# Kernel tuning notes

Hardware: AMD Instinct MI355X
Metric: run time of the kernel (lower is better)

Reference implementation:

```python
import jax, jax.numpy as jnp
import numpy as np

DIM = 2048
NUM_HEADS = 16
HEAD_DIM = 128
INNER = NUM_HEADS * HEAD_DIM


def rotate_half(x):
    x1, x2 = jnp.split(x, 2, axis=-1)
    return jnp.concatenate([-x2, x1], axis=-1)


def rope_tables(T, head_dim):
    inv_freq = 1.0 / (10000.0 ** (np.arange(0, head_dim, 2, dtype=np.float32) / head_dim))
    t = np.arange(T, dtype=np.float32)
    freqs = np.einsum('i,j->ij', t, inv_freq)  # [T, hd/2]
    emb = np.concatenate([freqs, freqs], axis=-1)  # [T, hd]
    return jnp.asarray(np.cos(emb)), jnp.asarray(np.sin(emb))


def setup_inputs() -> dict:
    key = jax.random.key(0)
    k1, k2, k3 = jax.random.split(key, 3)
    B, T = 2, 2048
    x = jax.random.normal(k1, (B, T, DIM), dtype=jnp.float32)
    scale = 1.0 / np.sqrt(DIM)
    w_qkv = jax.random.normal(k2, (DIM, 3 * INNER), dtype=jnp.float32) * scale
    w_out = jax.random.normal(k3, (INNER, DIM), dtype=jnp.float32) * (1.0 / np.sqrt(INNER))
    return {"x": x, "w_qkv": w_qkv, "w_out": w_out}


def reference(x, w_qkv, w_out):
    B, T, _ = x.shape
    qkv = x @ w_qkv  # [B, T, 3*INNER]
    q, k, v = jnp.split(qkv, 3, axis=-1)
    # [B, H, T, hd]
    q = q.reshape(B, T, NUM_HEADS, HEAD_DIM).transpose(0, 2, 1, 3)
    k = k.reshape(B, T, NUM_HEADS, HEAD_DIM).transpose(0, 2, 1, 3)
    v = v.reshape(B, T, NUM_HEADS, HEAD_DIM).transpose(0, 2, 1, 3)
    cos, sin = rope_tables(T, HEAD_DIM)  # [T, hd]
    cos = cos[None, None]
    sin = sin[None, None]
    q = q * cos + rotate_half(q) * sin
    k = k * cos + rotate_half(k) * sin
    # causal SDPA
    scale = 1.0 / np.sqrt(HEAD_DIM)
    scores = jnp.einsum('bhqd,bhkd->bhqk', q, k) * scale
    mask = jnp.tril(jnp.ones((T, T), dtype=bool))
    scores = jnp.where(mask[None, None], scores, jnp.finfo(scores.dtype).min)
    attn = jax.nn.softmax(scores, axis=-1)
    out = jnp.einsum('bhqk,bhkd->bhqd', attn, v)
    out = out.transpose(0, 2, 1, 3).reshape(B, T, INNER)
    return out @ w_out
```

## Files before the change

kernel.cpp:

```cpp
#include <hip/hip_runtime.h>
#include <hip/hip_bf16.h>
#include <math.h>

typedef __bf16 bf16x8 __attribute__((ext_vector_type(8)));
typedef float f32x4 __attribute__((ext_vector_type(4)));
typedef unsigned short ushort8_t __attribute__((ext_vector_type(8)));

#define DIMSZ 2048
#define NHEADS 16
#define HD 128
#define INNER 2048
#define T_SEQ 2048
#define BATCH 2
#define BT_ROWS (BATCH * T_SEQ)
#define QKV_COLS (3 * INNER)

__device__ __forceinline__ float bf2f(unsigned short u) {
  union { unsigned int ui; float f; } v; v.ui = ((unsigned int)u) << 16; return v.f;
}
__device__ __forceinline__ unsigned short f2bf(float f) {
  union { float f; unsigned int ui; } v; v.f = f;
  unsigned int u = v.ui;
  return (unsigned short)((u + 0x7FFFu + ((u >> 16) & 1u)) >> 16);
}
__device__ __forceinline__ bf16x8 ld8(const unsigned short* p) {
  return *(const bf16x8*)p;
}
__device__ __forceinline__ void gl16(const unsigned short* g, unsigned short* l) {
  __builtin_amdgcn_global_load_lds(
      (const __attribute__((address_space(1))) unsigned int*)g,
      (__attribute__((address_space(3))) unsigned int*)l, 16, 0, 0);
}

__global__ void detect_dtype(const unsigned short* __restrict__ w, int* __restrict__ flag) {
  __shared__ int sh;
  if (threadIdx.x == 0) sh = 0;
  __syncthreads();
  int hit = 0;
  for (int i = threadIdx.x; i < 8192; i += 256) {
    unsigned int e = (w[i] >> 7) & 0xFF;
    if (e >= 0x7F) hit = 1;
  }
  if (hit) atomicOr(&sh, 1);
  __syncthreads();
  if (threadIdx.x == 0) *flag = sh;
}

__global__ void convert_x(const void* __restrict__ in, unsigned short* __restrict__ out,
                          const int* __restrict__ flag) {
  const bool f32 = (*flag != 0);
  size_t i = ((size_t)blockIdx.x * 256 + threadIdx.x) * 8;
  if (f32) {
    const float* inf = (const float*)in;
    float4 u0 = *(const float4*)&inf[i];
    float4 u1 = *(const float4*)&inf[i + 4];
    ushort8_t t;
    t[0] = f2bf(u0.x); t[1] = f2bf(u0.y); t[2] = f2bf(u0.z); t[3] = f2bf(u0.w);
    t[4] = f2bf(u1.x); t[5] = f2bf(u1.y); t[6] = f2bf(u1.z); t[7] = f2bf(u1.w);
    *(ushort8_t*)&out[i] = t;
  } else {
    *(uint4*)&out[i] = *(const uint4*)&((const unsigned short*)in)[i];
  }
}

__global__ void transpose_any(const void* __restrict__ in, unsigned short* __restrict__ out,
                              int R, int C, const int* __restrict__ flag) {
  const bool f32 = (*flag != 0);
  __shared__ unsigned short tile[32][33];
  int c0 = blockIdx.x * 32, r0 = blockIdx.y * 32;
  int tx = threadIdx.x & 31, ty = threadIdx.x >> 5;
  if (f32) {
    const float* inf = (const float*)in;
    #pragma unroll
    for (int i = 0; i < 4; ++i)
      tile[ty + i * 8][tx] = f2bf(inf[(size_t)(r0 + ty + i * 8) * C + c0 + tx]);
  } else {
    const unsigned short* inu = (const unsigned short*)in;
    #pragma unroll
    for (int i = 0; i < 4; ++i)
      tile[ty + i * 8][tx] = inu[(size_t)(r0 + ty + i * 8) * C + c0 + tx];
  }
  __syncthreads();
  #pragma unroll
  for (int i = 0; i < 4; ++i)
    out[(size_t)(c0 + ty + i * 8) * R + r0 + tx] = tile[tx][ty + i * 8];
}

__global__ __launch_bounds__(256) void gemm_lds(const unsigned short* __restrict__ A,
                                                const unsigned short* __restrict__ Bt,
                                                unsigned short* __restrict__ Cb,
                                                float* __restrict__ Cf,
                                                int M, int N, int K) {
  __shared__ unsigned short As[128 * 32];
  __shared__ unsigned short Bs[128 * 32];
  const int tid = threadIdx.x;
  const int m0 = blockIdx.y * 128, n0 = blockIdx.x * 128;
  const int w = tid >> 6, L = tid & 63, lane = tid & 63, c = lane & 15, quad = lane >> 4;
  const int wm = (w & 1) * 64, wn = (w >> 1) * 64;
  f32x4 acc[4][4];
  #pragma unroll
  for (int i = 0; i < 4; ++i)
    #pragma unroll
    for (int j = 0; j < 4; ++j) acc[i][j] = (f32x4)0.0f;

  for (int k0 = 0; k0 < K; k0 += 32) {
    #pragma unroll
    for (int p = 0; p < 2; ++p) {
      int ci = p * 256 + w * 64 + L;
      int r = ci >> 2, s = ci & 3;
      gl16(&A[(size_t)(m0 + r) * K + k0 + s * 8], &As[(size_t)(p * 256 + w * 64) * 8]);
      gl16(&Bt[(size_t)(n0 + r) * K + k0 + s * 8], &Bs[(size_t)(p * 256 + w * 64) * 8]);
    }
    __syncthreads();
    bf16x8 af[4], bfr[4];
    #pragma unroll
    for (int i = 0; i < 4; ++i) af[i] = ld8(&As[(wm + i * 16 + c) * 32 + quad * 8]);
    #pragma unroll
    for (int j = 0; j < 4; ++j) bfr[j] = ld8(&Bs[(wn + j * 16 + c) * 32 + quad * 8]);
    #pragma unroll
    for (int i = 0; i < 4; ++i)
      #pragma unroll
      for (int j = 0; j < 4; ++j)
        acc[i][j] = __builtin_amdgcn_mfma_f32_16x16x32_bf16(af[i], bfr[j], acc[i][j], 0, 0, 0);
    __syncthreads();
  }
  if (Cf) {
    #pragma unroll
    for (int i = 0; i < 4; ++i)
      #pragma unroll
      for (int j = 0; j < 4; ++j)
        #pragma unroll
        for (int r = 0; r < 4; ++r)
          Cf[(size_t)(m0 + wm + i * 16 + quad * 4 + r) * N + n0 + wn + j * 16 + c] = acc[i][j][r];
  } else {
    #pragma unroll
    for (int i = 0; i < 4; ++i)
      #pragma unroll
      for (int j = 0; j < 4; ++j)
        #pragma unroll
        for (int r = 0; r < 4; ++r)
          Cb[(size_t)(m0 + wm + i * 16 + quad * 4 + r) * N + n0 + wn + j * 16 + c] =
              f2bf(acc[i][j][r]);
  }
}

__global__ void rope_kernel(unsigned short* __restrict__ qkv) {
  int idx = blockIdx.x * 256 + threadIdx.x;
  int jb = (idx & 7) * 8;
  int head = (idx >> 3) & 15;
  int qk = (idx >> 7) & 1;
  int row = idx >> 8;
  int t = row & (T_SEQ - 1);
  size_t base = (size_t)row * QKV_COLS + qk * INNER + head * HD + jb;
  ushort8_t x1 = *(ushort8_t*)&qkv[base];
  ushort8_t x2 = *(ushort8_t*)&qkv[base + 64];
  ushort8_t o1, o2;
  #pragma unroll
  for (int e = 0; e < 8; ++e) {
    float inv_freq = exp2f(-(float)(jb + e) * 0.20762050593046017f);
    float ang = (float)t * inv_freq;
    float sn = sinf(ang), cs = cosf(ang);
    float a = bf2f(x1[e]), bq = bf2f(x2[e]);
    o1[e] = f2bf(a * cs - bq * sn);
    o2[e] = f2bf(bq * cs + a * sn);
  }
  *(ushort8_t*)&qkv[base] = o1;
  *(ushort8_t*)&qkv[base + 64] = o2;
}

#define KT 64
#define KSTR 136
#define VSTR 72
#define PSTR 72
__global__ __launch_bounds__(256) void flash_attn2(const unsigned short* __restrict__ qkv,
                                                   unsigned short* __restrict__ aout) {
  __shared__ unsigned short Ks[KT * KSTR];
  __shared__ unsigned short Vs[HD * VSTR];
  __shared__ unsigned short Ps[4 * 16 * PSTR];
  const int tid = threadIdx.x, wave = tid >> 6, lane = tid & 63, c = lane & 15, quad = lane >> 4;
  const int bh = blockIdx.y, b = bh >> 4, h = bh & 15;
  unsigned short* myPs = &Ps[wave * 16 * PSTR];
  const unsigned short* qbase = qkv + (size_t)b * T_SEQ * QKV_COLS + h * HD;
  const unsigned short* kbase = qbase + INNER;
  const unsigned short* vbase = qbase + 2 * INNER;
  const float cf = 0.12751743f;

  for (int half = 0; half < 2; ++half) {
    const int qt = (half == 0) ? (int)blockIdx.x : 31 - (int)blockIdx.x;
    const int q0 = qt * 64;
    const int qrow = q0 + wave * 16;

    bf16x8 aq[4];
    #pragma unroll
    for (int ch = 0; ch < 4; ++ch)
      aq[ch] = ld8(&qbase[(size_t)(qrow + c) * QKV_COLS + ch * 32 + quad * 8]);

    f32x4 o[8];
    #pragma unroll
    for (int t = 0; t < 8; ++t) o[t] = (f32x4)0.0f;
    float l_part[4] = {0.f, 0.f, 0.f, 0.f};

    const int nkt = qt + 1;
    for (int it = 0; it < nkt; ++it) {
      const int kt = it * KT;
      __syncthreads();
      #pragma unroll
      for (int p = 0; p < 4; ++p) {
        int ci = p * 256 + tid;
        int r = ci >> 4, s = ci & 15;
        *(uint4*)&Ks[r * KSTR + s * 8] = *(const uint4*)&kbase[(size_t)(kt + r) * QKV_COLS + s * 8];
      }
      {
        int rp = tid & 31, seg = tid >> 5;
        const unsigned short* vp = &vbase[(size_t)(kt + 2 * rp) * QKV_COLS + seg * 16];
        ushort8_t v0a = *(const ushort8_t*)vp;
        ushort8_t v0b = *(const ushort8_t*)(vp + 8);
        ushort8_t v1a = *(const ushort8_t*)(vp + QKV_COLS);
        ushort8_t v1b = *(const ushort8_t*)(vp + QKV_COLS + 8);
        #pragma unroll
        for (int e = 0; e < 8; ++e) {
          *(unsigned int*)&Vs[(seg * 16 + e) * VSTR + 2 * rp] =
              (unsigned int)v0a[e] | ((unsigned int)v1a[e] << 16);
          *(unsigned int*)&Vs[(seg * 16 + 8 + e) * VSTR + 2 * rp] =
              (unsigned int)v0b[e] | ((unsigned int)v1b[e] << 16);
        }
      }
      __syncthreads();

      f32x4 s[4];
      #pragma unroll
      for (int st = 0; st < 4; ++st) s[st] = (f32x4)0.0f;
      #pragma unroll
      for (int ch = 0; ch < 4; ++ch) {
        #pragma unroll
        for (int st = 0; st < 4; ++st) {
          bf16x8 kf = ld8(&Ks[(st * 16 + c) * KSTR + ch * 32 + quad * 8]);
          s[st] = __builtin_amdgcn_mfma_f32_16x16x32_bf16(aq[ch], kf, s[st], 0, 0, 0);
        }
      }
      #pragma unroll
      for (int st = 0; st < 4; ++st) {
        #pragma unroll
        for (int r = 0; r < 4; ++r) {
          int qg = qrow + quad * 4 + r;
          int kg = kt + st * 16 + c;
          float p = (kg <= qg) ? exp2f(s[st][r] * cf) : 0.0f;
          l_part[r] += p;
          myPs[(quad * 4 + r) * PSTR + st * 16 + c] = f2bf(p);
        }
      }
      __syncthreads();
      bf16x8 pf0 = ld8(&myPs[c * PSTR + quad * 8]);
      bf16x8 pf1 = ld8(&myPs[c * PSTR + 32 + quad * 8]);
      #pragma unroll
      for (int t = 0; t < 8; ++t) {
        bf16x8 vf0 = ld8(&Vs[(t * 16 + c) * VSTR + quad * 8]);
        bf16x8 vf1 = ld8(&Vs[(t * 16 + c) * VSTR + 32 + quad * 8]);
        o[t] = __builtin_amdgcn_mfma_f32_16x16x32_bf16(pf0, vf0, o[t], 0, 0, 0);
        o[t] = __builtin_amdgcn_mfma_f32_16x16x32_bf16(pf1, vf1, o[t], 0, 0, 0);
      }
    }
    float inv[4];
    #pragma unroll
    for (int r = 0; r < 4; ++r) {
      float v = l_part[r];
      #pragma unroll
      for (int off = 1; off <= 8; off <<= 1) v += __shfl_xor(v, off, 64);
      inv[r] = 1.0f / v;
    }
    #pragma unroll
    for (int t = 0; t < 8; ++t)
      #pragma unroll
      for (int r = 0; r < 4; ++r)
        aout[(size_t)((size_t)b * T_SEQ + qrow + quad * 4 + r) * INNER + h * HD + t * 16 + c] =
            f2bf(o[t][r] * inv[r]);
  }
}

extern "C" void kernel_launch(void* const* d_in, const int* in_sizes, int n_in,
                              void* d_out, int out_size, void* d_ws, size_t ws_size,
                              hipStream_t stream) {
  const void* x     = d_in[0];
  const void* w_qkv = d_in[1];
  const void* w_out = d_in[2];
  float* out = (float*)d_out;

  int* flag = (int*)d_ws;
  unsigned short* qkvbuf  = (unsigned short*)((char*)d_ws + 256);
  unsigned short* attnout = qkvbuf + (size_t)BT_ROWS * QKV_COLS;
  unsigned short* wqkvT   = attnout + (size_t)BT_ROWS * INNER;
  unsigned short* woutT   = wqkvT + (size_t)QKV_COLS * DIMSZ;
  unsigned short* xb      = woutT + (size_t)DIMSZ * INNER;

  detect_dtype<<<1, 256, 0, stream>>>((const unsigned short*)w_qkv, flag);
  convert_x<<<dim3((size_t)BT_ROWS * DIMSZ / 2048), 256, 0, stream>>>(x, xb, flag);
  transpose_any<<<dim3(QKV_COLS / 32, DIMSZ / 32), 256, 0, stream>>>(w_qkv, wqkvT, DIMSZ, QKV_COLS, flag);
  transpose_any<<<dim3(DIMSZ / 32, INNER / 32), 256, 0, stream>>>(w_out, woutT, INNER, DIMSZ, flag);
  gemm_lds<<<dim3(QKV_COLS / 128, BT_ROWS / 128), 256, 0, stream>>>(xb, wqkvT, qkvbuf, nullptr, BT_ROWS, QKV_COLS, DIMSZ);
  rope_kernel<<<dim3(BT_ROWS * NHEADS * 2 * 8 / 256), 256, 0, stream>>>(qkvbuf);
  flash_attn2<<<dim3(16, BATCH * NHEADS), 256, 0, stream>>>(qkvbuf, attnout);
  gemm_lds<<<dim3(DIMSZ / 128, BT_ROWS / 128), 256, 0, stream>>>(attnout, woutT, nullptr, out, BT_ROWS, DIMSZ, INNER);
}
```

Baseline: 474.3 us.

## Rewrite flash attention with 32x32 MFMA tiles and split-K wave partitioning

Replaces the 16x16x32 MFMA attention kernel with one using 32x32x16 MFMAs, where the four waves form a 2x2 grid over query rows and key halves of each 64-key tile. Partial outputs and row sums from the two key-half waves are combined through shared memory at the end. The goal is fewer MFMA instructions and less LDS fragment traffic per tile, and removing the per-tile barrier before the P·V step. The cost is an extra reduction pass through LDS and more accumulator registers, with the launch bound set to 2 blocks.

```diff
diff --git a/kernel.cpp b/kernel.cpp
--- a/kernel.cpp
+++ b/kernel.cpp
@@ -4,7 +4,9 @@
 
 typedef __bf16 bf16x8 __attribute__((ext_vector_type(8)));
 typedef float f32x4 __attribute__((ext_vector_type(4)));
+typedef float f32x16 __attribute__((ext_vector_type(16)));
 typedef unsigned short ushort8_t __attribute__((ext_vector_type(8)));
+typedef unsigned short ushort4_t __attribute__((ext_vector_type(4)));
 
 #define DIMSZ 2048
 #define NHEADS 16
@@ -168,18 +170,27 @@
   *(ushort8_t*)&qkv[base + 64] = o2;
 }
 
-#define KT 64
-#define KSTR 136
-#define VSTR 72
-#define PSTR 72
-__global__ __launch_bounds__(256) void flash_attn2(const unsigned short* __restrict__ qkv,
-                                                   unsigned short* __restrict__ aout) {
-  __shared__ unsigned short Ks[KT * KSTR];
-  __shared__ unsigned short Vs[HD * VSTR];
-  __shared__ unsigned short Ps[4 * 16 * PSTR];
-  const int tid = threadIdx.x, wave = tid >> 6, lane = tid & 63, c = lane & 15, quad = lane >> 4;
+#define KT3 64
+#define KSTR3 136
+#define VSTR3 72
+#define PSTR3 68
+#define SM_VS (64 * KSTR3 * 2)
+#define SM_PS (SM_VS + 128 * VSTR3 * 2)
+#define SM_LR (SM_PS + 64 * PSTR3 * 2)
+#define SM_TOT (SM_LR + 2 * 64 * 4)
+__global__ __launch_bounds__(256, 2) void flash_attn3(const unsigned short* __restrict__ qkv,
+                                                      unsigned short* __restrict__ aout) {
+  __shared__ char smem[SM_TOT];
+  unsigned short* Ks = (unsigned short*)smem;
+  unsigned short* Vs = (unsigned short*)(smem + SM_VS);
+  unsigned short* Ps = (unsigned short*)(smem + SM_PS);
+  float* lred = (float*)(smem + SM_LR);
+  float* Os = (float*)smem;
+
+  const int tid = threadIdx.x, wave = tid >> 6, lane = tid & 63;
+  const int wq = wave & 1, wk = wave >> 1;
+  const int l31 = lane & 31, lh = lane >> 5;
   const int bh = blockIdx.y, b = bh >> 4, h = bh & 15;
-  unsigned short* myPs = &Ps[wave * 16 * PSTR];
   const unsigned short* qbase = qkv + (size_t)b * T_SEQ * QKV_COLS + h * HD;
   const unsigned short* kbase = qbase + INNER;
   const unsigned short* vbase = qbase + 2 * INNER;
@@ -188,27 +199,26 @@
   for (int half = 0; half < 2; ++half) {
     const int qt = (half == 0) ? (int)blockIdx.x : 31 - (int)blockIdx.x;
     const int q0 = qt * 64;
-    const int qrow = q0 + wave * 16;
-
-    bf16x8 aq[4];
-    #pragma unroll
-    for (int ch = 0; ch < 4; ++ch)
-      aq[ch] = ld8(&qbase[(size_t)(qrow + c) * QKV_COLS + ch * 32 + quad * 8]);
-
-    f32x4 o[8];
-    #pragma unroll
-    for (int t = 0; t < 8; ++t) o[t] = (f32x4)0.0f;
-    float l_part[4] = {0.f, 0.f, 0.f, 0.f};
+    const int qg = q0 + wq * 32 + l31;
+
+    bf16x8 aq[8];
+    #pragma unroll
+    for (int ch = 0; ch < 8; ++ch)
+      aq[ch] = ld8(&qbase[(size_t)qg * QKV_COLS + ch * 16 + lh * 8]);
+
+    f32x16 o[4];
+    #pragma unroll
+    for (int dt = 0; dt < 4; ++dt) o[dt] = (f32x16)0.0f;
+    float l_part = 0.0f;
 
     const int nkt = qt + 1;
     for (int it = 0; it < nkt; ++it) {
-      const int kt = it * KT;
+      const int kt = it * KT3;
       __syncthreads();
       #pragma unroll
       for (int p = 0; p < 4; ++p) {
-        int ci = p * 256 + tid;
-        int r = ci >> 4, s = ci & 15;
-        *(uint4*)&Ks[r * KSTR + s * 8] = *(const uint4*)&kbase[(size_t)(kt + r) * QKV_COLS + s * 8];
+        int ci = p * 256 + tid, r = ci >> 4, s = ci & 15;
+        *(uint4*)&Ks[r * KSTR3 + s * 8] = *(const uint4*)&kbase[(size_t)(kt + r) * QKV_COLS + s * 8];
       }
       {
         int rp = tid & 31, seg = tid >> 5;
@@ -219,61 +229,88 @@
         ushort8_t v1b = *(const ushort8_t*)(vp + QKV_COLS + 8);
         #pragma unroll
         for (int e = 0; e < 8; ++e) {
-          *(unsigned int*)&Vs[(seg * 16 + e) * VSTR + 2 * rp] =
+          *(unsigned int*)&Vs[(seg * 16 + e) * VSTR3 + 2 * rp] =
               (unsigned int)v0a[e] | ((unsigned int)v1a[e] << 16);
-          *(unsigned int*)&Vs[(seg * 16 + 8 + e) * VSTR + 2 * rp] =
+          *(unsigned int*)&Vs[(seg * 16 + 8 + e) * VSTR3 + 2 * rp] =
               (unsigned int)v0b[e] | ((unsigned int)v1b[e] << 16);
         }
       }
       __syncthreads();
 
-      f32x4 s[4];
-      #pragma unroll
-      for (int st = 0; st < 4; ++st) s[st] = (f32x4)0.0f;
-      #pragma unroll
-      for (int ch = 0; ch < 4; ++ch) {
-        #pragma unroll
-        for (int st = 0; st < 4; ++st) {
-          bf16x8 kf = ld8(&Ks[(st * 16 + c) * KSTR + ch * 32 + quad * 8]);
-          s[st] = __builtin_amdgcn_mfma_f32_16x16x32_bf16(aq[ch], kf, s[st], 0, 0, 0);
-        }
-      }
-      #pragma unroll
-      for (int st = 0; st < 4; ++st) {
-        #pragma unroll
-        for (int r = 0; r < 4; ++r) {
-          int qg = qrow + quad * 4 + r;
-          int kg = kt + st * 16 + c;
-          float p = (kg <= qg) ? exp2f(s[st][r] * cf) : 0.0f;
-          l_part[r] += p;
-          myPs[(quad * 4 + r) * PSTR + st * 16 + c] = f2bf(p);
-        }
-      }
-      __syncthreads();
-      bf16x8 pf0 = ld8(&myPs[c * PSTR + quad * 8]);
-      bf16x8 pf1 = ld8(&myPs[c * PSTR + 32 + quad * 8]);
-      #pragma unroll
-      for (int t = 0; t < 8; ++t) {
-        bf16x8 vf0 = ld8(&Vs[(t * 16 + c) * VSTR + quad * 8]);
-        bf16x8 vf1 = ld8(&Vs[(t * 16 + c) * VSTR + 32 + quad * 8]);
-        o[t] = __builtin_amdgcn_mfma_f32_16x16x32_bf16(pf0, vf0, o[t], 0, 0, 0);
-        o[t] = __builtin_amdgcn_mfma_f32_16x16x32_bf16(pf1, vf1, o[t], 0, 0, 0);
+      f32x16 st = (f32x16)0.0f;
+      #pragma unroll
+      for (int ch = 0; ch < 8; ++ch) {
+        bf16x8 kf = ld8(&Ks[(wk * 32 + l31) * KSTR3 + ch * 16 + lh * 8]);
+        st = __builtin_amdgcn_mfma_f32_32x32x16_bf16(kf, aq[ch], st, 0, 0, 0);
+      }
+      unsigned short* prow = &Ps[(wq * 32 + l31) * PSTR3 + wk * 32];
+      #pragma unroll
+      for (int g = 0; g < 4; ++g) {
+        ushort4_t pk;
+        #pragma unroll
+        for (int e = 0; e < 4; ++e) {
+          int r = g * 4 + e;
+          int keyl = e + 8 * g + 4 * lh;
+          int kg = kt + wk * 32 + keyl;
+          float p = (kg <= qg) ? exp2f(st[r] * cf) : 0.0f;
+          l_part += p;
+          pk[e] = f2bf(p);
+        }
+        *(ushort4_t*)&prow[g * 8 + 4 * lh] = pk;
+      }
+      bf16x8 pf[2];
+      #pragma unroll
+      for (int kc = 0; kc < 2; ++kc) {
+        uint2 pa = *(const uint2*)&Ps[(wq * 32 + l31) * PSTR3 + wk * 32 + kc * 16 + lh * 8];
+        uint2 pb = *(const uint2*)&Ps[(wq * 32 + l31) * PSTR3 + wk * 32 + kc * 16 + lh * 8 + 4];
+        union { uint4 u; bf16x8 v; } cvt;
+        cvt.u.x = pa.x; cvt.u.y = pa.y; cvt.u.z = pb.x; cvt.u.w = pb.y;
+        pf[kc] = cvt.v;
+      }
+      #pragma unroll
+      for (int dt = 0; dt < 4; ++dt) {
+        #pragma unroll
+        for (int kc = 0; kc < 2; ++kc) {
+          bf16x8 vf = ld8(&Vs[(dt * 32 + l31) * VSTR3 + wk * 32 + kc * 16 + lh * 8]);
+          o[dt] = __builtin_amdgcn_mfma_f32_32x32x16_bf16(pf[kc], vf, o[dt], 0, 0, 0);
+        }
       }
     }
-    float inv[4];
-    #pragma unroll
-    for (int r = 0; r < 4; ++r) {
-      float v = l_part[r];
-      #pragma unroll
-      for (int off = 1; off <= 8; off <<= 1) v += __shfl_xor(v, off, 64);
-      inv[r] = 1.0f / v;
+
+    float lv = l_part + __shfl_xor(l_part, 32, 64);
+    __syncthreads();
+    if (lane < 32) lred[wk * 64 + wq * 32 + lane] = lv;
+    if (wk == 1) {
+      #pragma unroll
+      for (int dt = 0; dt < 4; ++dt)
+        #pragma unroll
+        for (int s = 0; s < 4; ++s) {
+          f32x4 seg4 = {o[dt][s * 4 + 0], o[dt][s * 4 + 1], o[dt][s * 4 + 2], o[dt][s * 4 + 3]};
+          *(f32x4*)&Os[(size_t)(wq * 64 + lane) * 68 + dt * 16 + s * 4] = seg4;
+        }
     }
-    #pragma unroll
-    for (int t = 0; t < 8; ++t)
-      #pragma unroll
-      for (int r = 0; r < 4; ++r)
-        aout[(size_t)((size_t)b * T_SEQ + qrow + quad * 4 + r) * INNER + h * HD + t * 16 + c] =
-            f2bf(o[t][r] * inv[r]);
+    __syncthreads();
+    if (wk == 0) {
+      float invr[16];
+      #pragma unroll
+      for (int r = 0; r < 16; ++r) {
+        int ql = wq * 32 + (r & 3) + 8 * (r >> 2) + 4 * lh;
+        invr[r] = 1.0f / (lred[ql] + lred[64 + ql]);
+      }
+      #pragma unroll
+      for (int dt = 0; dt < 4; ++dt) {
+        f32x4 add[4];
+        #pragma unroll
+        for (int s = 0; s < 4; ++s)
+          add[s] = *(const f32x4*)&Os[(size_t)(wq * 64 + lane) * 68 + dt * 16 + s * 4];
+        #pragma unroll
+        for (int r = 0; r < 16; ++r) {
+          float val = (o[dt][r] + add[r >> 2][r & 3]) * invr[r];
+          int qrow = q0 + wq * 32 + (r & 3) + 8 * (r >> 2) + 4 * lh;
+          aout[(size_t)((size_t)b * T_SEQ + qrow) * INNER + h * HD + dt * 32 + l31] = f2bf(val);
+        }
+      }
+    }
   }
 }
 
@@ -298,6 +335,6 @@
   transpose_any<<<dim3(DIMSZ / 32, INNER / 32), 256, 0, stream>>>(w_out, woutT, INNER, DIMSZ, flag);
   gemm_lds<<<dim3(QKV_COLS / 128, BT_ROWS / 128), 256, 0, stream>>>(xb, wqkvT, qkvbuf, nullptr, BT_ROWS, QKV_COLS, DIMSZ);
   rope_kernel<<<dim3(BT_ROWS * NHEADS * 2 * 8 / 256), 256, 0, stream>>>(qkvbuf);
-  flash_attn2<<<dim3(16, BATCH * NHEADS), 256, 0, stream>>>(qkvbuf, attnout);
+  flash_attn3<<<dim3(16, BATCH * NHEADS), 256, 0, stream>>>(qkvbuf, attnout);
   gemm_lds<<<dim3(DIMSZ / 128, BT_ROWS / 128), 256, 0, stream>>>(attnout, woutT, nullptr, out, BT_ROWS, DIMSZ, INNER);
 }
```

Result: faster. 451.6 us (-4.8%).
